# Optimization experiments

Measured on AMD Instinct MI355X. Metric: run time of the kernel, lower is better.

The kernel has to match this reference:

```python
import jax, jax.numpy as jnp
import numpy as np

HOP = 128
NFFT = 256
SR = 16000
EPS = 1e-7
MIN_DB = -80.0


def _a_weighting_db():
    # librosa.fft_frequencies + librosa.A_weighting (min_db=-80), computed statically in numpy
    f = np.fft.rfftfreq(NFFT, d=1.0 / SR)  # [NFFT//2+1]
    c = np.array([12194.217, 20.598997, 107.65265, 737.86223]) ** 2.0
    f2 = f ** 2.0
    w = 2.0 + 20.0 * (
        np.log10(c[0])
        + 2.0 * np.log10(np.maximum(f2, 1e-30))
        - np.log10(f2 + c[0])
        - np.log10(f2 + c[1])
        - 0.5 * np.log10(f2 + c[2])
        - 0.5 * np.log10(f2 + c[3])
    )
    return np.maximum(w, MIN_DB).astype(np.float32)


def _loudness(x):
    # x: [B, C, T] -> channel mean -> librosa-style centered STFT (hann, reflect pad)
    x = jnp.mean(x, axis=1)  # [B, T]
    T = x.shape[1]
    pad = NFFT // 2
    xp = jnp.pad(x, ((0, 0), (pad, pad)), mode='reflect')  # [B, T+NFFT]
    n_frames = 1 + T // HOP
    idx = jnp.arange(n_frames)[:, None] * HOP + jnp.arange(NFFT)[None, :]  # [F, NFFT]
    frames = xp[:, idx]  # [B, F, NFFT]
    # periodic hann window (scipy fftbins=True, librosa default)
    win = (0.5 - 0.5 * jnp.cos(2.0 * jnp.pi * jnp.arange(NFFT) / NFFT)).astype(x.dtype)
    spec = jnp.fft.rfft(frames * win, axis=-1)  # [B, F, NFFT//2+1] complex
    log_mag = jnp.log(jnp.abs(spec) + EPS)  # [B, F, NFREQ]
    aw = jnp.asarray(_a_weighting_db())  # [NFREQ]
    # mean over frequency axis, then trailing singleton like original unsqueeze(-1)
    loud = jnp.mean(log_mag + aw[None, None, :], axis=-1)  # [B, F]
    return loud[..., None].astype(jnp.float32)


def setup_inputs() -> dict:
    key = jax.random.key(0)
    x = jax.random.normal(key, (64, 1, 640000), dtype=jnp.float32)
    return {"x": x}


def reference(x):
    return _loudness(x)
```

## Files before the change

kernel.cpp:

```cpp
#include <hip/hip_runtime.h>
#include <math.h>

#define HOP 128
#define T_LEN 640000
#define N_FRAMES 5001
#define N_PAIRS 2501
#define NB 64
#define GPB 16

#define RE_SLOT 18
#define RE_GRP  160
#define IM_SLOT 18
#define IM_GRP  142

typedef float v2f __attribute__((ext_vector_type(2)));

static __device__ __forceinline__ v2f mk2(float a, float b) { v2f r; r.x = a; r.y = b; return r; }
static __device__ __forceinline__ v2f sp(float s) { v2f r; r.x = s; r.y = s; return r; }

static __device__ __forceinline__ float rsum16(float v) {
    v += __int_as_float(__builtin_amdgcn_update_dpp(0, __float_as_int(v), 0xB1, 0xF, 0xF, true));
    v += __int_as_float(__builtin_amdgcn_update_dpp(0, __float_as_int(v), 0x4E, 0xF, 0xF, true));
    v += __int_as_float(__builtin_amdgcn_update_dpp(0, __float_as_int(v), 0x141, 0xF, 0xF, true));
    v += __int_as_float(__builtin_amdgcn_update_dpp(0, __float_as_int(v), 0x140, 0xF, 0xF, true));
    return v;
}

__global__ __launch_bounds__(256) void loudness_kernel(const float* __restrict__ x,
                                                       float* __restrict__ out) {
    constexpr float C16[16] = {
        1.0f,  0.9238795325112867f,  0.7071067811865476f,  0.3826834323650898f,
        0.0f, -0.3826834323650898f, -0.7071067811865476f, -0.9238795325112867f,
       -1.0f, -0.9238795325112867f, -0.7071067811865476f, -0.3826834323650898f,
        0.0f,  0.3826834323650898f,  0.7071067811865476f,  0.9238795325112867f};
    constexpr float S16[16] = {
        0.0f,  0.3826834323650898f,  0.7071067811865476f,  0.9238795325112867f,
        1.0f,  0.9238795325112867f,  0.7071067811865476f,  0.3826834323650898f,
        0.0f, -0.3826834323650898f, -0.7071067811865476f, -0.9238795325112867f,
       -1.0f, -0.9238795325112867f, -0.7071067811865476f, -0.3826834323650898f};
    const float R2  = 0.7071067811865476f;
    const float c1v = 0.9238795325112867f, s1v = 0.3826834323650898f;
    const float c3v = 0.3826834323650898f, s3v = 0.9238795325112867f;
    const float CP8 = 0.9238795325112867f, SP8 = 0.3826834323650898f;
    const float K2  = 1.8477590650225735f;

    __shared__ alignas(16) v2f s_re[16 * RE_GRP];
    __shared__ alignas(16) v2f s_im[16 * IM_GRP];
    __shared__ v2f   s_stp[16];
    __shared__ float s_aw8[16];
    __shared__ float s_aw128;

    const int tid = threadIdx.x;

    {
        const float TP = 0.02454369260617026f;
        if (tid < 16) {
            float s, c;
            sincosf((float)tid * TP, &s, &c);
            s_stp[tid] = mk2(c, -s);
        }
        if (tid < 129) {
            float fq = (float)tid * 62.5f;
            float f2 = fq * fq;
            const float a0 = 12194.217f * 12194.217f;
            const float a1 = 20.598997f * 20.598997f;
            const float a2 = 107.65265f * 107.65265f;
            const float a3 = 737.86223f * 737.86223f;
            float w = 2.0f + 20.0f * (log10f(a0) + 2.0f * log10f(fmaxf(f2, 1e-30f))
                     - log10f(f2 + a0) - log10f(f2 + a1)
                     - 0.5f * log10f(f2 + a2) - 0.5f * log10f(f2 + a3));
            ((float*)&s_im[0])[tid] = fmaxf(w, -80.0f);
        }
    }
    __syncthreads();
    if (tid < 16) {
        const float* scr = (const float*)&s_im[0];
        float s = 0.f;
#pragma unroll
        for (int k2 = 0; k2 < 8; ++k2) s += scr[tid + 16 * k2];
        s_aw8[tid] = s;
        if (tid == 0) s_aw128 = scr[128];
    }
    __syncthreads();
    s_im[(tid >> 4) * IM_GRP + (tid & 15)] = sp(0.f);
    __syncthreads();

    const int g  = tid >> 4;
    const int r  = tid & 15;
    const int gp = blockIdx.x * GPB + g;
    const int b  = gp / N_PAIRS;
    const int pp = gp - b * N_PAIRS;
    const int fA = 2 * pp;
    const int fB = (fA < 5000) ? fA + 1 : 5000;
    const int dB = (fB - fA) * HOP;
    const float* __restrict__ xb = x + (size_t)b * T_LEN;

    const v2f stp = s_stp[r];
    float win16[16];
    {
        float cm2 = stp.x;
        float cm1 = stp.x * CP8 + stp.y * SP8;
        win16[0] = 0.5f - 0.5f * cm2;
        win16[1] = 0.5f - 0.5f * cm1;
#pragma unroll
        for (int n = 2; n < 16; ++n) {
            const float c = K2 * cm1 - cm2;
            win16[n] = 0.5f - 0.5f * c;
            cm2 = cm1; cm1 = c;
        }
    }

    v2f xw[16];
    const int base = fA * HOP - HOP + r;
    if (pp >= 1 && pp <= 2499) {
        const float* __restrict__ xp = xb + base;
#pragma unroll
        for (int n2 = 0; n2 < 16; ++n2) {
            const int o = 16 * n2;
            xw[n2] = mk2(xp[o], xp[o + dB]) * sp(win16[n2]);
        }
    } else {
#pragma unroll
        for (int n2 = 0; n2 < 16; ++n2) {
            int jA = base + 16 * n2;
            int jB = jA + dB;
            jA = (jA < 0) ? -jA : jA;
            jA = (jA >= T_LEN) ? (2 * T_LEN - 2 - jA) : jA;
            jB = (jB < 0) ? -jB : jB;
            jB = (jB >= T_LEN) ? (2 * T_LEN - 2 - jB) : jB;
            xw[n2] = mk2(xb[jA], xb[jB]) * sp(win16[n2]);
        }
    }

    v2f p[8], q[8];
#pragma unroll
    for (int n = 1; n <= 7; ++n) { p[n] = xw[n] + xw[16 - n]; q[n] = xw[n] - xw[16 - n]; }
    const v2f bse = xw[0] + xw[8];
    const v2f d08 = xw[0] - xw[8];
    const v2f se  = p[2] + p[4] + p[6];
    const v2f so  = p[1] + p[3] + p[5] + p[7];
    const v2f r0  = bse + se + so;
    const v2f r8  = bse + se - so;
    v2f rre[8], rim[8];
#pragma unroll
    for (int k1 = 1; k1 <= 7; ++k1) {
        v2f re = (k1 & 1) ? d08 : bse;
        v2f im = sp(0.f);
#pragma unroll
        for (int n = 1; n <= 7; ++n) {
            const int m = (k1 * n) & 15;
            re += p[n] * sp(C16[m]);
            im -= q[n] * sp(S16[m]);
        }
        rre[k1] = re;
        rim[k1] = im;
    }

    {
        v2f* __restrict__ reW = &s_re[g * RE_GRP + r];
        v2f* __restrict__ imW = &s_im[g * IM_GRP + r];
        reW[0] = r0;
#pragma unroll
        for (int k = 1; k <= 7; ++k) {
            reW[RE_SLOT * k] = rre[k];
            imW[IM_SLOT * k] = rim[k];
        }
        reW[RE_SLOT * 8] = r8;
    }

    const int rp  = (r <= 8) ? r : 16 - r;
    const int rp7 = rp & 7;
    const v2f sgnv = sp((r <= 8) ? 1.f : -1.f);
    const float4* __restrict__ reCol = (const float4*)&s_re[g * RE_GRP + RE_SLOT * rp];
    const float4* __restrict__ imCol = (const float4*)&s_im[g * IM_GRP + IM_SLOT * rp7];

    v2f bbx[16], bby[16];
    float tc = 1.f, tms = 0.f;
    const float sc = stp.x, sms = stp.y;
#pragma unroll
    for (int j = 0; j < 8; ++j) {
        const float4 R4v = reCol[j];
        const float4 I4v = imCol[j];
        {
            const v2f xx = mk2(R4v.x, R4v.y);
            const v2f yy = mk2(I4v.x, I4v.y) * sgnv;
            if (j == 0) { bbx[0] = xx; bby[0] = yy; }
            else {
                bbx[2 * j] = xx * sp(tc) - yy * sp(tms);
                bby[2 * j] = xx * sp(tms) + yy * sp(tc);
            }
            const float ntc = tc * sc - tms * sms;
            const float nts = tc * sms + tms * sc;
            tc = ntc; tms = nts;
        }
        {
            const v2f xx = mk2(R4v.z, R4v.w);
            const v2f yy = mk2(I4v.z, I4v.w) * sgnv;
            bbx[2 * j + 1] = xx * sp(tc) - yy * sp(tms);
            bby[2 * j + 1] = xx * sp(tms) + yy * sp(tc);
            if (j < 7) {
                const float ntc = tc * sc - tms * sms;
                const float nts = tc * sms + tms * sc;
                tc = ntc; tms = nts;
            }
        }
    }

#pragma unroll
    for (int j = 0; j < 8; ++j) {
        const v2f ux = bbx[j], uy = bby[j], vx = bbx[j + 8], vy = bby[j + 8];
        bbx[j] = ux + vx; bby[j] = uy + vy;
        const v2f dx = ux - vx, dy = uy - vy;
        v2f ox, oy;
        if      (j == 0) { ox = dx;                              oy = dy; }
        else if (j == 1) { ox =  dx * sp(c1v) + dy * sp(s1v);    oy =  dy * sp(c1v) - dx * sp(s1v); }
        else if (j == 2) { ox = (dx + dy) * sp(R2);              oy = (dy - dx) * sp(R2); }
        else if (j == 3) { ox =  dx * sp(c3v) + dy * sp(s3v);    oy =  dy * sp(c3v) - dx * sp(s3v); }
        else if (j == 4) { ox = dy;                              oy = sp(0.f) - dx; }
        else if (j == 5) { ox = dy * sp(s3v) - dx * sp(c3v);     oy = sp(0.f) - dy * sp(c3v) - dx * sp(s3v); }
        else if (j == 6) { ox = (dy - dx) * sp(R2);              oy = sp(0.f) - (dx + dy) * sp(R2); }
        else             { ox = dy * sp(s1v) - dx * sp(c1v);     oy = sp(0.f) - dy * sp(c1v) - dx * sp(s1v); }
        bbx[j + 8] = ox; bby[j + 8] = oy;
    }
#pragma unroll
    for (int h = 0; h <= 8; h += 8) {
#pragma unroll
        for (int j = 0; j < 4; ++j) {
            const v2f ux = bbx[h + j], uy = bby[h + j], vx = bbx[h + j + 4], vy = bby[h + j + 4];
            bbx[h + j] = ux + vx; bby[h + j] = uy + vy;
            const v2f dx = ux - vx, dy = uy - vy;
            v2f ox, oy;
            if      (j == 0) { ox = dx;                  oy = dy; }
            else if (j == 1) { ox = (dx + dy) * sp(R2);  oy = (dy - dx) * sp(R2); }
            else if (j == 2) { ox = dy;                  oy = sp(0.f) - dx; }
            else             { ox = (dy - dx) * sp(R2);  oy = sp(0.f) - (dx + dy) * sp(R2); }
            bbx[h + j + 4] = ox; bby[h + j + 4] = oy;
        }
    }
#pragma unroll
    for (int gg = 0; gg < 16; gg += 4) {
        {
            const v2f ux = bbx[gg], uy = bby[gg], vx = bbx[gg + 2], vy = bby[gg + 2];
            bbx[gg] = ux + vx;     bby[gg] = uy + vy;
            bbx[gg + 2] = ux - vx; bby[gg + 2] = uy - vy;
        }
        {
            const v2f ux = bbx[gg + 1], uy = bby[gg + 1], vx = bbx[gg + 3], vy = bby[gg + 3];
            bbx[gg + 1] = ux + vx; bby[gg + 1] = uy + vy;
            const v2f dx = ux - vx, dy = uy - vy;
            bbx[gg + 3] = dy; bby[gg + 3] = sp(0.f) - dx;
        }
    }

    const float HALF_LN2 = 0.34657359027997264f;
    v2f m2[8];
#pragma unroll
    for (int t = 0; t < 8; ++t) {
        const v2f Yx = bbx[2 * t] + bbx[2 * t + 1];
        const v2f Yy = bby[2 * t] + bby[2 * t + 1];
        m2[t] = Yx * Yx + Yy * Yy + sp(1e-14f);
    }
    const v2f P0 = m2[0] * m2[1], P1 = m2[2] * m2[3], P2 = m2[4] * m2[5], P3 = m2[6] * m2[7];
    const float lA = __builtin_amdgcn_logf(P0.x) + __builtin_amdgcn_logf(P1.x)
                   + __builtin_amdgcn_logf(P2.x) + __builtin_amdgcn_logf(P3.x);
    const float lB = __builtin_amdgcn_logf(P0.y) + __builtin_amdgcn_logf(P1.y)
                   + __builtin_amdgcn_logf(P2.y) + __builtin_amdgcn_logf(P3.y);
    v2f ssum = sp(HALF_LN2) * mk2(lA, lB) + sp(s_aw8[r]);

    const v2f d0 = bbx[0] - bbx[1];
    if (r == 0) {
        ssum += sp(HALF_LN2) * mk2(__builtin_amdgcn_logf(d0.x * d0.x + 1e-14f),
                                   __builtin_amdgcn_logf(d0.y * d0.y + 1e-14f))
              + sp(s_aw128);
    }

    ssum.x = rsum16(ssum.x);
    ssum.y = rsum16(ssum.y);

    if (r == 0) {
        out[b * N_FRAMES + fA] = ssum.x * (1.0f / 129.0f);
        out[b * N_FRAMES + fB] = ssum.y * (1.0f / 129.0f);
    }
}

extern "C" void kernel_launch(void* const* d_in, const int* in_sizes, int n_in,
                              void* d_out, int out_size, void* d_ws, size_t ws_size,
                              hipStream_t stream) {
    const float* x = (const float*)d_in[0];
    float* out = (float*)d_out;
    loudness_kernel<<<(NB * N_PAIRS) / GPB, 256, 0, stream>>>(x, out);
}
```

Measured before the change: 57.14 us.

## Process multiple frame pairs per thread group to amortize block setup

Each 16-thread group now loops over four frame pairs instead of one, cutting the grid by four so the per-block setup (sincos, A-weighting table, syncs, window) is amortized. Twiddle factors are precomputed once per thread into a register array instead of being recurred inside each FFT pass. Shared-memory group strides are padded, and the A-weighting setup uses a hardware log2 with scaling instead of log10f. Fewer blocks mean fewer waves in flight to hide memory latency, and the loop carries no intra-group sync between iterations, which relies on wave-level ordering of the shared-memory reuse.

```diff
diff --git a/kernel.cpp b/kernel.cpp
--- a/kernel.cpp
+++ b/kernel.cpp
@@ -7,11 +7,13 @@
 #define N_PAIRS 2501
 #define NB 64
 #define GPB 16
+#define MP 4
+#define NBLK 2501
 
 #define RE_SLOT 18
-#define RE_GRP  160
+#define RE_GRP  164
 #define IM_SLOT 18
-#define IM_GRP  142
+#define IM_GRP  146
 
 typedef float v2f __attribute__((ext_vector_type(2)));
 
@@ -60,15 +62,17 @@
             s_stp[tid] = mk2(c, -s);
         }
         if (tid < 129) {
+            const float LG2_10 = 0.30102999566398f;
             float fq = (float)tid * 62.5f;
             float f2 = fq * fq;
             const float a0 = 12194.217f * 12194.217f;
             const float a1 = 20.598997f * 20.598997f;
             const float a2 = 107.65265f * 107.65265f;
             const float a3 = 737.86223f * 737.86223f;
-            float w = 2.0f + 20.0f * (log10f(a0) + 2.0f * log10f(fmaxf(f2, 1e-30f))
-                     - log10f(f2 + a0) - log10f(f2 + a1)
-                     - 0.5f * log10f(f2 + a2) - 0.5f * log10f(f2 + a3));
+            float w = 2.0f + 20.0f * LG2_10 *
+                      (__builtin_amdgcn_logf(a0) + 2.0f * __builtin_amdgcn_logf(fmaxf(f2, 1e-30f))
+                     - __builtin_amdgcn_logf(f2 + a0) - __builtin_amdgcn_logf(f2 + a1)
+                     - 0.5f * __builtin_amdgcn_logf(f2 + a2) - 0.5f * __builtin_amdgcn_logf(f2 + a3));
             ((float*)&s_im[0])[tid] = fmaxf(w, -80.0f);
         }
     }
@@ -85,17 +89,22 @@
     s_im[(tid >> 4) * IM_GRP + (tid & 15)] = sp(0.f);
     __syncthreads();
 
-    const int g  = tid >> 4;
-    const int r  = tid & 15;
-    const int gp = blockIdx.x * GPB + g;
-    const int b  = gp / N_PAIRS;
-    const int pp = gp - b * N_PAIRS;
-    const int fA = 2 * pp;
-    const int fB = (fA < 5000) ? fA + 1 : 5000;
-    const int dB = (fB - fA) * HOP;
-    const float* __restrict__ xb = x + (size_t)b * T_LEN;
-
-    const v2f stp = s_stp[r];
+    const int g = tid >> 4;
+    const int r = tid & 15;
+
+    const v2f   stp   = s_stp[r];
+    const float aw8r  = s_aw8[r];
+    const float aw128 = s_aw128;
+
+    v2f twr[16];
+    twr[0] = mk2(1.f, 0.f);
+    twr[1] = stp;
+#pragma unroll
+    for (int w = 2; w < 16; ++w) {
+        const v2f t = twr[w - 1];
+        twr[w] = mk2(t.x * stp.x - t.y * stp.y, t.x * stp.y + t.y * stp.x);
+    }
+
     float win16[16];
     {
         float cm2 = stp.x;
@@ -110,55 +119,73 @@
         }
     }
 
-    v2f xw[16];
-    const int base = fA * HOP - HOP + r;
-    if (pp >= 1 && pp <= 2499) {
-        const float* __restrict__ xp = xb + base;
-#pragma unroll
-        for (int n2 = 0; n2 < 16; ++n2) {
-            const int o = 16 * n2;
-            xw[n2] = mk2(xp[o], xp[o + dB]) * sp(win16[n2]);
-        }
-    } else {
-#pragma unroll
-        for (int n2 = 0; n2 < 16; ++n2) {
-            int jA = base + 16 * n2;
-            int jB = jA + dB;
-            jA = (jA < 0) ? -jA : jA;
-            jA = (jA >= T_LEN) ? (2 * T_LEN - 2 - jA) : jA;
-            jB = (jB < 0) ? -jB : jB;
-            jB = (jB >= T_LEN) ? (2 * T_LEN - 2 - jB) : jB;
-            xw[n2] = mk2(xb[jA], xb[jB]) * sp(win16[n2]);
-        }
-    }
-
-    v2f p[8], q[8];
-#pragma unroll
-    for (int n = 1; n <= 7; ++n) { p[n] = xw[n] + xw[16 - n]; q[n] = xw[n] - xw[16 - n]; }
-    const v2f bse = xw[0] + xw[8];
-    const v2f d08 = xw[0] - xw[8];
-    const v2f se  = p[2] + p[4] + p[6];
-    const v2f so  = p[1] + p[3] + p[5] + p[7];
-    const v2f r0  = bse + se + so;
-    const v2f r8  = bse + se - so;
-    v2f rre[8], rim[8];
-#pragma unroll
-    for (int k1 = 1; k1 <= 7; ++k1) {
-        v2f re = (k1 & 1) ? d08 : bse;
-        v2f im = sp(0.f);
-#pragma unroll
-        for (int n = 1; n <= 7; ++n) {
-            const int m = (k1 * n) & 15;
-            re += p[n] * sp(C16[m]);
-            im -= q[n] * sp(S16[m]);
-        }
-        rre[k1] = re;
-        rim[k1] = im;
-    }
-
-    {
-        v2f* __restrict__ reW = &s_re[g * RE_GRP + r];
-        v2f* __restrict__ imW = &s_im[g * IM_GRP + r];
+    const int rp  = (r <= 8) ? r : 16 - r;
+    const int rp7 = rp & 7;
+    const v2f sgnv = sp((r <= 8) ? 1.f : -1.f);
+    v2f* __restrict__ reW = &s_re[g * RE_GRP + r];
+    v2f* __restrict__ imW = &s_im[g * IM_GRP + r];
+    const float4* __restrict__ reCol = (const float4*)&s_re[g * RE_GRP + RE_SLOT * rp];
+    const float4* __restrict__ imCol = (const float4*)&s_im[g * IM_GRP + IM_SLOT * rp7];
+
+    const int p0 = (blockIdx.x * GPB + g) * MP;
+    const float HALF_LN2 = 0.34657359027997264f;
+
+#pragma unroll 1
+    for (int it = 0; it < MP; ++it) {
+        const int p  = p0 + it;
+        const int b  = p / N_PAIRS;
+        const int pp = p - b * N_PAIRS;
+        const int fA = 2 * pp;
+        const int fB = (fA < 5000) ? fA + 1 : 5000;
+        const int dB = (fB - fA) * HOP;
+        const float* __restrict__ xb = x + (size_t)b * T_LEN;
+
+        v2f xw[16];
+        const int base = fA * HOP - HOP + r;
+        if (pp >= 1 && pp <= 2499) {
+            const float* __restrict__ xp = xb + base;
+#pragma unroll
+            for (int n2 = 0; n2 < 16; ++n2) {
+                const int o = 16 * n2;
+                xw[n2] = mk2(xp[o], xp[o + dB]) * sp(win16[n2]);
+            }
+        } else {
+#pragma unroll
+            for (int n2 = 0; n2 < 16; ++n2) {
+                int jA = base + 16 * n2;
+                int jB = jA + dB;
+                jA = (jA < 0) ? -jA : jA;
+                jA = (jA >= T_LEN) ? (2 * T_LEN - 2 - jA) : jA;
+                jB = (jB < 0) ? -jB : jB;
+                jB = (jB >= T_LEN) ? (2 * T_LEN - 2 - jB) : jB;
+                xw[n2] = mk2(xb[jA], xb[jB]) * sp(win16[n2]);
+            }
+        }
+
+        v2f pv[8], qv[8];
+#pragma unroll
+        for (int n = 1; n <= 7; ++n) { pv[n] = xw[n] + xw[16 - n]; qv[n] = xw[n] - xw[16 - n]; }
+        const v2f bse = xw[0] + xw[8];
+        const v2f d08 = xw[0] - xw[8];
+        const v2f se  = pv[2] + pv[4] + pv[6];
+        const v2f so  = pv[1] + pv[3] + pv[5] + pv[7];
+        const v2f r0  = bse + se + so;
+        const v2f r8  = bse + se - so;
+        v2f rre[8], rim[8];
+#pragma unroll
+        for (int k1 = 1; k1 <= 7; ++k1) {
+            v2f re = (k1 & 1) ? d08 : bse;
+            v2f im = sp(0.f);
+#pragma unroll
+            for (int n = 1; n <= 7; ++n) {
+                const int m = (k1 * n) & 15;
+                re += pv[n] * sp(C16[m]);
+                im -= qv[n] * sp(S16[m]);
+            }
+            rre[k1] = re;
+            rim[k1] = im;
+        }
+
         reW[0] = r0;
 #pragma unroll
         for (int k = 1; k <= 7; ++k) {
@@ -166,120 +193,105 @@
             imW[IM_SLOT * k] = rim[k];
         }
         reW[RE_SLOT * 8] = r8;
-    }
-
-    const int rp  = (r <= 8) ? r : 16 - r;
-    const int rp7 = rp & 7;
-    const v2f sgnv = sp((r <= 8) ? 1.f : -1.f);
-    const float4* __restrict__ reCol = (const float4*)&s_re[g * RE_GRP + RE_SLOT * rp];
-    const float4* __restrict__ imCol = (const float4*)&s_im[g * IM_GRP + IM_SLOT * rp7];
-
-    v2f bbx[16], bby[16];
-    float tc = 1.f, tms = 0.f;
-    const float sc = stp.x, sms = stp.y;
-#pragma unroll
-    for (int j = 0; j < 8; ++j) {
-        const float4 R4v = reCol[j];
-        const float4 I4v = imCol[j];
-        {
-            const v2f xx = mk2(R4v.x, R4v.y);
-            const v2f yy = mk2(I4v.x, I4v.y) * sgnv;
-            if (j == 0) { bbx[0] = xx; bby[0] = yy; }
-            else {
-                bbx[2 * j] = xx * sp(tc) - yy * sp(tms);
-                bby[2 * j] = xx * sp(tms) + yy * sp(tc);
-            }
-            const float ntc = tc * sc - tms * sms;
-            const float nts = tc * sms + tms * sc;
-            tc = ntc; tms = nts;
-        }
-        {
-            const v2f xx = mk2(R4v.z, R4v.w);
-            const v2f yy = mk2(I4v.z, I4v.w) * sgnv;
-            bbx[2 * j + 1] = xx * sp(tc) - yy * sp(tms);
-            bby[2 * j + 1] = xx * sp(tms) + yy * sp(tc);
-            if (j < 7) {
-                const float ntc = tc * sc - tms * sms;
-                const float nts = tc * sms + tms * sc;
-                tc = ntc; tms = nts;
-            }
-        }
-    }
-
-#pragma unroll
-    for (int j = 0; j < 8; ++j) {
-        const v2f ux = bbx[j], uy = bby[j], vx = bbx[j + 8], vy = bby[j + 8];
-        bbx[j] = ux + vx; bby[j] = uy + vy;
-        const v2f dx = ux - vx, dy = uy - vy;
-        v2f ox, oy;
-        if      (j == 0) { ox = dx;                              oy = dy; }
-        else if (j == 1) { ox =  dx * sp(c1v) + dy * sp(s1v);    oy =  dy * sp(c1v) - dx * sp(s1v); }
-        else if (j == 2) { ox = (dx + dy) * sp(R2);              oy = (dy - dx) * sp(R2); }
-        else if (j == 3) { ox =  dx * sp(c3v) + dy * sp(s3v);    oy =  dy * sp(c3v) - dx * sp(s3v); }
-        else if (j == 4) { ox = dy;                              oy = sp(0.f) - dx; }
-        else if (j == 5) { ox = dy * sp(s3v) - dx * sp(c3v);     oy = sp(0.f) - dy * sp(c3v) - dx * sp(s3v); }
-        else if (j == 6) { ox = (dy - dx) * sp(R2);              oy = sp(0.f) - (dx + dy) * sp(R2); }
-        else             { ox = dy * sp(s1v) - dx * sp(c1v);     oy = sp(0.f) - dy * sp(c1v) - dx * sp(s1v); }
-        bbx[j + 8] = ox; bby[j + 8] = oy;
-    }
-#pragma unroll
-    for (int h = 0; h <= 8; h += 8) {
-#pragma unroll
-        for (int j = 0; j < 4; ++j) {
-            const v2f ux = bbx[h + j], uy = bby[h + j], vx = bbx[h + j + 4], vy = bby[h + j + 4];
-            bbx[h + j] = ux + vx; bby[h + j] = uy + vy;
+
+        v2f bbx[16], bby[16];
+#pragma unroll
+        for (int j = 0; j < 8; ++j) {
+            const float4 R4v = reCol[j];
+            const float4 I4v = imCol[j];
+            {
+                const int w = 2 * j;
+                const v2f xx = mk2(R4v.x, R4v.y);
+                const v2f yy = mk2(I4v.x, I4v.y) * sgnv;
+                if (j == 0) { bbx[0] = xx; bby[0] = yy; }
+                else {
+                    bbx[w] = xx * sp(twr[w].x) - yy * sp(twr[w].y);
+                    bby[w] = xx * sp(twr[w].y) + yy * sp(twr[w].x);
+                }
+            }
+            {
+                const int w = 2 * j + 1;
+                const v2f xx = mk2(R4v.z, R4v.w);
+                const v2f yy = mk2(I4v.z, I4v.w) * sgnv;
+                bbx[w] = xx * sp(twr[w].x) - yy * sp(twr[w].y);
+                bby[w] = xx * sp(twr[w].y) + yy * sp(twr[w].x);
+            }
+        }
+
+#pragma unroll
+        for (int j = 0; j < 8; ++j) {
+            const v2f ux = bbx[j], uy = bby[j], vx = bbx[j + 8], vy = bby[j + 8];
+            bbx[j] = ux + vx; bby[j] = uy + vy;
             const v2f dx = ux - vx, dy = uy - vy;
             v2f ox, oy;
-            if      (j == 0) { ox = dx;                  oy = dy; }
-            else if (j == 1) { ox = (dx + dy) * sp(R2);  oy = (dy - dx) * sp(R2); }
-            else if (j == 2) { ox = dy;                  oy = sp(0.f) - dx; }
-            else             { ox = (dy - dx) * sp(R2);  oy = sp(0.f) - (dx + dy) * sp(R2); }
-            bbx[h + j + 4] = ox; bby[h + j + 4] = oy;
-        }
-    }
-#pragma unroll
-    for (int gg = 0; gg < 16; gg += 4) {
-        {
-            const v2f ux = bbx[gg], uy = bby[gg], vx = bbx[gg + 2], vy = bby[gg + 2];
-            bbx[gg] = ux + vx;     bby[gg] = uy + vy;
-            bbx[gg + 2] = ux - vx; bby[gg + 2] = uy - vy;
-        }
-        {
-            const v2f ux = bbx[gg + 1], uy = bby[gg + 1], vx = bbx[gg + 3], vy = bby[gg + 3];
-            bbx[gg + 1] = ux + vx; bby[gg + 1] = uy + vy;
-            const v2f dx = ux - vx, dy = uy - vy;
-            bbx[gg + 3] = dy; bby[gg + 3] = sp(0.f) - dx;
-        }
-    }
-
-    const float HALF_LN2 = 0.34657359027997264f;
-    v2f m2[8];
-#pragma unroll
-    for (int t = 0; t < 8; ++t) {
-        const v2f Yx = bbx[2 * t] + bbx[2 * t + 1];
-        const v2f Yy = bby[2 * t] + bby[2 * t + 1];
-        m2[t] = Yx * Yx + Yy * Yy + sp(1e-14f);
-    }
-    const v2f P0 = m2[0] * m2[1], P1 = m2[2] * m2[3], P2 = m2[4] * m2[5], P3 = m2[6] * m2[7];
-    const float lA = __builtin_amdgcn_logf(P0.x) + __builtin_amdgcn_logf(P1.x)
-                   + __builtin_amdgcn_logf(P2.x) + __builtin_amdgcn_logf(P3.x);
-    const float lB = __builtin_amdgcn_logf(P0.y) + __builtin_amdgcn_logf(P1.y)
-                   + __builtin_amdgcn_logf(P2.y) + __builtin_amdgcn_logf(P3.y);
-    v2f ssum = sp(HALF_LN2) * mk2(lA, lB) + sp(s_aw8[r]);
-
-    const v2f d0 = bbx[0] - bbx[1];
-    if (r == 0) {
-        ssum += sp(HALF_LN2) * mk2(__builtin_amdgcn_logf(d0.x * d0.x + 1e-14f),
-                                   __builtin_amdgcn_logf(d0.y * d0.y + 1e-14f))
-              + sp(s_aw128);
-    }
-
-    ssum.x = rsum16(ssum.x);
-    ssum.y = rsum16(ssum.y);
-
-    if (r == 0) {
-        out[b * N_FRAMES + fA] = ssum.x * (1.0f / 129.0f);
-        out[b * N_FRAMES + fB] = ssum.y * (1.0f / 129.0f);
+            if      (j == 0) { ox = dx;                              oy = dy; }
+            else if (j == 1) { ox =  dx * sp(c1v) + dy * sp(s1v);    oy =  dy * sp(c1v) - dx * sp(s1v); }
+            else if (j == 2) { ox = (dx + dy) * sp(R2);              oy = (dy - dx) * sp(R2); }
+            else if (j == 3) { ox =  dx * sp(c3v) + dy * sp(s3v);    oy =  dy * sp(c3v) - dx * sp(s3v); }
+            else if (j == 4) { ox = dy;                              oy = sp(0.f) - dx; }
+            else if (j == 5) { ox = dy * sp(s3v) - dx * sp(c3v);     oy = sp(0.f) - dy * sp(c3v) - dx * sp(s3v); }
+            else if (j == 6) { ox = (dy - dx) * sp(R2);              oy = sp(0.f) - (dx + dy) * sp(R2); }
+            else             { ox = dy * sp(s1v) - dx * sp(c1v);     oy = sp(0.f) - dy * sp(c1v) - dx * sp(s1v); }
+            bbx[j + 8] = ox; bby[j + 8] = oy;
+        }
+#pragma unroll
+        for (int h = 0; h <= 8; h += 8) {
+#pragma unroll
+            for (int j = 0; j < 4; ++j) {
+                const v2f ux = bbx[h + j], uy = bby[h + j], vx = bbx[h + j + 4], vy = bby[h + j + 4];
+                bbx[h + j] = ux + vx; bby[h + j] = uy + vy;
+                const v2f dx = ux - vx, dy = uy - vy;
+                v2f ox, oy;
+                if      (j == 0) { ox = dx;                  oy = dy; }
+                else if (j == 1) { ox = (dx + dy) * sp(R2);  oy = (dy - dx) * sp(R2); }
+                else if (j == 2) { ox = dy;                  oy = sp(0.f) - dx; }
+                else             { ox = (dy - dx) * sp(R2);  oy = sp(0.f) - (dx + dy) * sp(R2); }
+                bbx[h + j + 4] = ox; bby[h + j + 4] = oy;
+            }
+        }
+#pragma unroll
+        for (int gg = 0; gg < 16; gg += 4) {
+            {
+                const v2f ux = bbx[gg], uy = bby[gg], vx = bbx[gg + 2], vy = bby[gg + 2];
+                bbx[gg] = ux + vx;     bby[gg] = uy + vy;
+                bbx[gg + 2] = ux - vx; bby[gg + 2] = uy - vy;
+            }
+            {
+                const v2f ux = bbx[gg + 1], uy = bby[gg + 1], vx = bbx[gg + 3], vy = bby[gg + 3];
+                bbx[gg + 1] = ux + vx; bby[gg + 1] = uy + vy;
+                const v2f dx = ux - vx, dy = uy - vy;
+                bbx[gg + 3] = dy; bby[gg + 3] = sp(0.f) - dx;
+            }
+        }
+
+        v2f m2[8];
+#pragma unroll
+        for (int t = 0; t < 8; ++t) {
+            const v2f Yx = bbx[2 * t] + bbx[2 * t + 1];
+            const v2f Yy = bby[2 * t] + bby[2 * t + 1];
+            m2[t] = Yx * Yx + Yy * Yy + sp(1e-14f);
+        }
+        const v2f P0 = m2[0] * m2[1], P1 = m2[2] * m2[3], P2 = m2[4] * m2[5], P3 = m2[6] * m2[7];
+        const float lA = __builtin_amdgcn_logf(P0.x) + __builtin_amdgcn_logf(P1.x)
+                       + __builtin_amdgcn_logf(P2.x) + __builtin_amdgcn_logf(P3.x);
+        const float lB = __builtin_amdgcn_logf(P0.y) + __builtin_amdgcn_logf(P1.y)
+                       + __builtin_amdgcn_logf(P2.y) + __builtin_amdgcn_logf(P3.y);
+        v2f ssum = sp(HALF_LN2) * mk2(lA, lB) + sp(aw8r);
+
+        const v2f d0 = bbx[0] - bbx[1];
+        if (r == 0) {
+            ssum += sp(HALF_LN2) * mk2(__builtin_amdgcn_logf(d0.x * d0.x + 1e-14f),
+                                       __builtin_amdgcn_logf(d0.y * d0.y + 1e-14f))
+                  + sp(aw128);
+        }
+
+        ssum.x = rsum16(ssum.x);
+        ssum.y = rsum16(ssum.y);
+
+        if (r == 0) {
+            out[b * N_FRAMES + fA] = ssum.x * (1.0f / 129.0f);
+            out[b * N_FRAMES + fB] = ssum.y * (1.0f / 129.0f);
+        }
     }
 }
 
@@ -288,5 +300,5 @@
                               hipStream_t stream) {
     const float* x = (const float*)d_in[0];
     float* out = (float*)d_out;
-    loudness_kernel<<<(NB * N_PAIRS) / GPB, 256, 0, stream>>>(x, out);
+    loudness_kernel<<<NBLK, 256, 0, stream>>>(x, out);
 }
```

Measured after the change: 61.22 us. +7.1%, slower.
